# Optimization experiments

Hardware: AMD Instinct MI355X
Metric: run time of the kernel (lower is better)

Reference implementation:

```python
import jax, jax.numpy as jnp
import numpy as np

IN_F, OUT_F, K_MAX = 4096, 4096, 512
B, S = 8, 2048


def setup_inputs() -> dict:
    key = jax.random.key(0)
    kx, ku, kv = jax.random.split(key, 3)
    x = jax.random.normal(kx, (B, S, IN_F), dtype=jnp.float32)
    # kaiming_uniform_ with a=sqrt(5): bound = sqrt(6 / ((1 + a^2) * fan_in)) = sqrt(1/fan_in)
    bu = 1.0 / np.sqrt(IN_F)
    bv = 1.0 / np.sqrt(OUT_F)
    U = jax.random.uniform(ku, (IN_F, K_MAX), minval=-bu, maxval=bu, dtype=jnp.float32)
    V = jax.random.uniform(kv, (OUT_F, K_MAX), minval=-bv, maxval=bv, dtype=jnp.float32)
    s = jnp.ones((K_MAX,), dtype=jnp.float32)
    mask = jnp.ones((K_MAX,), dtype=jnp.bool_)
    return {"x": x, "U": U, "V": V, "s": s, "mask": mask}


def reference(x, U, V, s, mask):
    # s_masked = s * mask; W = V @ diag(s_masked) @ U^T; out = x @ W^T
    s_masked = s * mask.astype(s.dtype)            # [k]
    W = (V * s_masked[None, :]) @ U.T              # [out, in] (V @ diag(s) fused as column scale)
    return jnp.einsum('bsi,oi->bso', x, W)         # F.linear(x, W)
```

## Files before the change

kernel.cpp:

```cpp
#include <hip/hip_runtime.h>
#include <hip/hip_bf16.h>
#include <stdint.h>


typedef __attribute__((ext_vector_type(8))) short short8;
typedef __attribute__((ext_vector_type(4))) float f32x4;
typedef __attribute__((ext_vector_type(4))) unsigned int uint4v;


__device__ __forceinline__ unsigned short f2bf_rne(float f) {
    unsigned int u = __builtin_bit_cast(unsigned int, f);
    unsigned int r = u + 0x7fffu + ((u >> 16) & 1u);
    return (unsigned short)(r >> 16);
}

__device__ __forceinline__ unsigned int pk2bf(float a, float b) {
    unsigned int ua = __builtin_bit_cast(unsigned int, a);
    unsigned int ub = __builtin_bit_cast(unsigned int, b);
    ua = (ua + 0x8000u) >> 16;
    ub = (ub + 0x8000u) & 0xffff0000u;
    return ua | ub;
}

__device__ __forceinline__ void async_load16(const void* g, void* l) {
    __builtin_amdgcn_global_load_lds(
        (const __attribute__((address_space(1))) unsigned int*)g,
        (__attribute__((address_space(3))) unsigned int*)l,
        16, 0, 0);
}


__global__ void prep_u(const float* __restrict__ U, const float* __restrict__ S,
                       const int* __restrict__ Mask, unsigned short* __restrict__ Ut) {
    __shared__ float t[32][33];
    const int tx = threadIdx.x, ty = threadIdx.y;
    const int n0 = blockIdx.x * 32, k0 = blockIdx.y * 32;
#pragma unroll
    for (int i = 0; i < 4; ++i)
        t[ty + i * 8][tx] = U[(size_t)(k0 + ty + i * 8) * 512 + n0 + tx];
    __syncthreads();
#pragma unroll
    for (int i = 0; i < 4; ++i) {
        int n = n0 + ty + i * 8;
        float sm = S[n] * (Mask[n] != 0 ? 1.0f : 0.0f);
        Ut[(size_t)n * 4096 + k0 + tx] = f2bf_rne(t[tx][ty + i * 8] * sm);
    }
}

__global__ void prep_v(const float* __restrict__ V, unsigned short* __restrict__ Vb) {
    int i = blockIdx.x * blockDim.x + threadIdx.x;
    float4 f = ((const float4*)V)[i];
    ushort4 o;
    o.x = f2bf_rne(f.x); o.y = f2bf_rne(f.y);
    o.z = f2bf_rne(f.z); o.w = f2bf_rne(f.w);
    ((ushort4*)Vb)[i] = o;
}

__global__ __launch_bounds__(256, 2)
void gemm1_xu(const float* __restrict__ X, const unsigned short* __restrict__ Ut,
              unsigned short* __restrict__ Y) {
    const int tid  = threadIdx.x;
    const int lane = tid & 63;
    const int w    = tid >> 6;
    const int ln   = lane & 15;
    const int quad = lane >> 4;
    const int m0 = blockIdx.y * 128;
    const int n0 = blockIdx.x * 128;
    const int wm = (w >> 1) * 64;
    const int wn = (w & 1) * 64;

    __shared__ short8 As[1024];
    __shared__ short8 Bs[1024];

    f32x4 acc[4][4] = {};

    for (int kt = 0; kt < 4096; kt += 64) {
        __syncthreads();
#pragma unroll
        for (int i = 0; i < 4; ++i) {
            int cbase = i * 256 + w * 64;
            int c = cbase + lane;
            int kc = c >> 7, n = c & 127;
            async_load16(Ut + (size_t)(n0 + n) * 4096 + kt + kc * 8, (void*)&Bs[cbase]);
        }
#pragma unroll
        for (int i = 0; i < 4; ++i) {
            int c = i * 256 + tid;
            int kc = c >> 7, m = c & 127;
            const float* src = X + (size_t)(m0 + m) * 4096 + kt + kc * 8;
            float4 f0 = *(const float4*)(src);
            float4 f1 = *(const float4*)(src + 4);
            uint4v p;
            p.x = pk2bf(f0.x, f0.y); p.y = pk2bf(f0.z, f0.w);
            p.z = pk2bf(f1.x, f1.y); p.w = pk2bf(f1.z, f1.w);
            As[c] = __builtin_bit_cast(short8, p);
        }
        __syncthreads();
#pragma unroll
        for (int ks = 0; ks < 2; ++ks) {
            const int kc = ks * 4 + quad;
            short8 a[4], b[4];
#pragma unroll
            for (int t = 0; t < 4; ++t) {
                a[t] = As[kc * 128 + wm + t * 16 + ln];
                b[t] = Bs[kc * 128 + wn + t * 16 + ln];
            }
#pragma unroll
            for (int mt = 0; mt < 4; ++mt)
#pragma unroll
                for (int nt = 0; nt < 4; ++nt)
                    acc[mt][nt] = __builtin_amdgcn_mfma_f32_16x16x32_bf16(
                        a[mt], b[nt], acc[mt][nt], 0, 0, 0);
        }
    }
#pragma unroll
    for (int mt = 0; mt < 4; ++mt)
#pragma unroll
        for (int nt = 0; nt < 4; ++nt) {
            int col = n0 + wn + nt * 16 + ln;
#pragma unroll
            for (int r = 0; r < 4; ++r) {
                int row = m0 + wm + mt * 16 + quad * 4 + r;
                Y[(size_t)row * 512 + col] = f2bf_rne(acc[mt][nt][r]);
            }
        }
}

__global__ __launch_bounds__(256, 2)
void gemm2_yv(const unsigned short* __restrict__ Y, const unsigned short* __restrict__ Vb,
              float* __restrict__ Out) {
    const int tid  = threadIdx.x;
    const int lane = tid & 63;
    const int w    = tid >> 6;
    const int ln   = lane & 15;
    const int quad = lane >> 4;
    const int m0 = blockIdx.y * 128;
    const int n0 = blockIdx.x * 128;
    const int wm = (w >> 1) * 64;
    const int wn = (w & 1) * 64;

    __shared__ short8 As[1024];
    __shared__ short8 Bs[1024];

    f32x4 acc[4][4] = {};

    for (int kt = 0; kt < 512; kt += 64) {
        __syncthreads();
#pragma unroll
        for (int i = 0; i < 4; ++i) {
            int cbase = i * 256 + w * 64;
            int c = cbase + lane;
            int kc = c >> 7, r = c & 127;
            async_load16(Y  + (size_t)(m0 + r) * 512 + kt + kc * 8, (void*)&As[cbase]);
            async_load16(Vb + (size_t)(n0 + r) * 512 + kt + kc * 8, (void*)&Bs[cbase]);
        }
        __syncthreads();
#pragma unroll
        for (int ks = 0; ks < 2; ++ks) {
            const int kc = ks * 4 + quad;
            short8 a[4], b[4];
#pragma unroll
            for (int t = 0; t < 4; ++t) {
                a[t] = As[kc * 128 + wm + t * 16 + ln];
                b[t] = Bs[kc * 128 + wn + t * 16 + ln];
            }
#pragma unroll
            for (int mt = 0; mt < 4; ++mt)
#pragma unroll
                for (int nt = 0; nt < 4; ++nt)
                    acc[mt][nt] = __builtin_amdgcn_mfma_f32_16x16x32_bf16(
                        a[mt], b[nt], acc[mt][nt], 0, 0, 0);
        }
    }
#pragma unroll
    for (int mt = 0; mt < 4; ++mt)
#pragma unroll
        for (int nt = 0; nt < 4; ++nt) {
            int col = n0 + wn + nt * 16 + ln;
#pragma unroll
            for (int r = 0; r < 4; ++r) {
                int row = m0 + wm + mt * 16 + quad * 4 + r;
                Out[(size_t)row * 4096 + col] = acc[mt][nt][r];
            }
        }
}


extern "C" void kernel_launch(void* const* d_in, const int* in_sizes, int n_in,
                              void* d_out, int out_size, void* d_ws, size_t ws_size,
                              hipStream_t stream) {
    const float* X    = (const float*)d_in[0];
    const float* U    = (const float*)d_in[1];
    const float* V    = (const float*)d_in[2];
    const float* S    = (const float*)d_in[3];
    const int*   Mask = (const int*)d_in[4];

    char* ws = (char*)d_ws;
    unsigned short* Ut = (unsigned short*)ws;
    unsigned short* Vb = (unsigned short*)(ws + (size_t)512 * 4096 * 2);
    unsigned short* Yb = (unsigned short*)(ws + (size_t)512 * 4096 * 4);
    float* Out = (float*)d_out;

    prep_u<<<dim3(16, 128), dim3(32, 8), 0, stream>>>(U, S, Mask, Ut);
    prep_v<<<dim3(1024), dim3(512), 0, stream>>>(V, Vb);
    gemm1_xu<<<dim3(4, 128), dim3(256), 0, stream>>>(X, Ut, Yb);
    gemm2_yv<<<dim3(32, 128), dim3(256), 0, stream>>>(Yb, Vb, Out);
}
```

Measured before the change: 759.6 us.

## Pre-convert X to bf16 and double-buffer LDS in a unified GEMM kernel

Adds a separate prep_x pass that converts the fp32 activations to bf16, so GEMM1 can load both operands with async global-to-LDS copies instead of converting X inside the main loop. Both GEMMs now share one templated kernel that double-buffers shared memory, issuing the next tile's loads before computing the current one. This removes one barrier per iteration and overlaps loads with MFMA work. The cost is an extra full read of X plus a 128 MB bf16 write and read, and twice the LDS per block. If the workspace is too small, the output buffer is reused as scratch for X.

```diff
diff --git a/kernel.cpp b/kernel.cpp
--- a/kernel.cpp
+++ b/kernel.cpp
@@ -56,9 +56,22 @@
     ((ushort4*)Vb)[i] = o;
 }
 
+__global__ __launch_bounds__(256) void prep_x(const float* __restrict__ X,
+                                              unsigned short* __restrict__ Xb) {
+    size_t i = (size_t)blockIdx.x * 256 + threadIdx.x;
+    const float4* src = (const float4*)X;
+    float4 f0 = src[2 * i];
+    float4 f1 = src[2 * i + 1];
+    uint4v p;
+    p.x = pk2bf(f0.x, f0.y); p.y = pk2bf(f0.z, f0.w);
+    p.z = pk2bf(f1.x, f1.y); p.w = pk2bf(f1.z, f1.w);
+    ((uint4v*)Xb)[i] = p;
+}
+
+template <int K, bool OUT_BF16, int LDOUT>
 __global__ __launch_bounds__(256, 2)
-void gemm1_xu(const float* __restrict__ X, const unsigned short* __restrict__ Ut,
-              unsigned short* __restrict__ Y) {
+void gemm_bt(const unsigned short* __restrict__ A, const unsigned short* __restrict__ B,
+             void* __restrict__ Out) {
     const int tid  = threadIdx.x;
     const int lane = tid & 63;
     const int w    = tid >> 6;
@@ -69,41 +82,38 @@
     const int wm = (w >> 1) * 64;
     const int wn = (w & 1) * 64;
 
-    __shared__ short8 As[1024];
-    __shared__ short8 Bs[1024];
+    __shared__ short8 As[2][1024];
+    __shared__ short8 Bs[2][1024];
 
     f32x4 acc[4][4] = {};
 
-    for (int kt = 0; kt < 4096; kt += 64) {
-        __syncthreads();
+    constexpr int NT = K / 64;
+
+    auto stage = [&](int buf, int kt) {
 #pragma unroll
         for (int i = 0; i < 4; ++i) {
             int cbase = i * 256 + w * 64;
             int c = cbase + lane;
-            int kc = c >> 7, n = c & 127;
-            async_load16(Ut + (size_t)(n0 + n) * 4096 + kt + kc * 8, (void*)&Bs[cbase]);
+            int kc = c >> 7, r = c & 127;
+            async_load16(A + (size_t)(m0 + r) * K + kt + kc * 8, (void*)&As[buf][cbase]);
+            async_load16(B + (size_t)(n0 + r) * K + kt + kc * 8, (void*)&Bs[buf][cbase]);
         }
-#pragma unroll
-        for (int i = 0; i < 4; ++i) {
-            int c = i * 256 + tid;
-            int kc = c >> 7, m = c & 127;
-            const float* src = X + (size_t)(m0 + m) * 4096 + kt + kc * 8;
-            float4 f0 = *(const float4*)(src);
-            float4 f1 = *(const float4*)(src + 4);
-            uint4v p;
-            p.x = pk2bf(f0.x, f0.y); p.y = pk2bf(f0.z, f0.w);
-            p.z = pk2bf(f1.x, f1.y); p.w = pk2bf(f1.z, f1.w);
-            As[c] = __builtin_bit_cast(short8, p);
-        }
+    };
+
+    stage(0, 0);
+    int cur = 0;
+#pragma unroll 1
+    for (int t = 0; t < NT; ++t) {
         __syncthreads();
+        if (t + 1 < NT) stage(cur ^ 1, (t + 1) * 64);
 #pragma unroll
         for (int ks = 0; ks < 2; ++ks) {
             const int kc = ks * 4 + quad;
             short8 a[4], b[4];
 #pragma unroll
-            for (int t = 0; t < 4; ++t) {
-                a[t] = As[kc * 128 + wm + t * 16 + ln];
-                b[t] = Bs[kc * 128 + wn + t * 16 + ln];
+            for (int tt = 0; tt < 4; ++tt) {
+                a[tt] = As[cur][kc * 128 + wm + tt * 16 + ln];
+                b[tt] = Bs[cur][kc * 128 + wn + tt * 16 + ln];
             }
 #pragma unroll
             for (int mt = 0; mt < 4; ++mt)
@@ -112,7 +122,9 @@
                     acc[mt][nt] = __builtin_amdgcn_mfma_f32_16x16x32_bf16(
                         a[mt], b[nt], acc[mt][nt], 0, 0, 0);
         }
+        cur ^= 1;
     }
+
 #pragma unroll
     for (int mt = 0; mt < 4; ++mt)
 #pragma unroll
@@ -121,66 +133,10 @@
 #pragma unroll
             for (int r = 0; r < 4; ++r) {
                 int row = m0 + wm + mt * 16 + quad * 4 + r;
-                Y[(size_t)row * 512 + col] = f2bf_rne(acc[mt][nt][r]);
-            }
-        }
-}
-
-__global__ __launch_bounds__(256, 2)
-void gemm2_yv(const unsigned short* __restrict__ Y, const unsigned short* __restrict__ Vb,
-              float* __restrict__ Out) {
-    const int tid  = threadIdx.x;
-    const int lane = tid & 63;
-    const int w    = tid >> 6;
-    const int ln   = lane & 15;
-    const int quad = lane >> 4;
-    const int m0 = blockIdx.y * 128;
-    const int n0 = blockIdx.x * 128;
-    const int wm = (w >> 1) * 64;
-    const int wn = (w & 1) * 64;
-
-    __shared__ short8 As[1024];
-    __shared__ short8 Bs[1024];
-
-    f32x4 acc[4][4] = {};
-
-    for (int kt = 0; kt < 512; kt += 64) {
-        __syncthreads();
-#pragma unroll
-        for (int i = 0; i < 4; ++i) {
-            int cbase = i * 256 + w * 64;
-            int c = cbase + lane;
-            int kc = c >> 7, r = c & 127;
-            async_load16(Y  + (size_t)(m0 + r) * 512 + kt + kc * 8, (void*)&As[cbase]);
-            async_load16(Vb + (size_t)(n0 + r) * 512 + kt + kc * 8, (void*)&Bs[cbase]);
-        }
-        __syncthreads();
-#pragma unroll
-        for (int ks = 0; ks < 2; ++ks) {
-            const int kc = ks * 4 + quad;
-            short8 a[4], b[4];
-#pragma unroll
-            for (int t = 0; t < 4; ++t) {
-                a[t] = As[kc * 128 + wm + t * 16 + ln];
-                b[t] = Bs[kc * 128 + wn + t * 16 + ln];
-            }
-#pragma unroll
-            for (int mt = 0; mt < 4; ++mt)
-#pragma unroll
-                for (int nt = 0; nt < 4; ++nt)
-                    acc[mt][nt] = __builtin_amdgcn_mfma_f32_16x16x32_bf16(
-                        a[mt], b[nt], acc[mt][nt], 0, 0, 0);
-        }
-    }
-#pragma unroll
-    for (int mt = 0; mt < 4; ++mt)
-#pragma unroll
-        for (int nt = 0; nt < 4; ++nt) {
-            int col = n0 + wn + nt * 16 + ln;
-#pragma unroll
-            for (int r = 0; r < 4; ++r) {
-                int row = m0 + wm + mt * 16 + quad * 4 + r;
-                Out[(size_t)row * 4096 + col] = acc[mt][nt][r];
+                if constexpr (OUT_BF16)
+                    ((unsigned short*)Out)[(size_t)row * LDOUT + col] = f2bf_rne(acc[mt][nt][r]);
+                else
+                    ((float*)Out)[(size_t)row * LDOUT + col] = acc[mt][nt][r];
             }
         }
 }
@@ -196,13 +152,25 @@
     const int*   Mask = (const int*)d_in[4];
 
     char* ws = (char*)d_ws;
+    const size_t UT_B = (size_t)512 * 4096 * 2;
+    const size_t VB_B = (size_t)512 * 4096 * 2;
+    const size_t YB_B = (size_t)16384 * 512 * 2;
+    const size_t XB_B = (size_t)16384 * 4096 * 2;
+
     unsigned short* Ut = (unsigned short*)ws;
-    unsigned short* Vb = (unsigned short*)(ws + (size_t)512 * 4096 * 2);
-    unsigned short* Yb = (unsigned short*)(ws + (size_t)512 * 4096 * 4);
+    unsigned short* Vb = (unsigned short*)(ws + UT_B);
+    unsigned short* Yb = (unsigned short*)(ws + UT_B + VB_B);
     float* Out = (float*)d_out;
+
+    unsigned short* Xb;
+    if (ws_size >= UT_B + VB_B + YB_B + XB_B)
+        Xb = (unsigned short*)(ws + UT_B + VB_B + YB_B);
+    else
+        Xb = (unsigned short*)d_out;
 
     prep_u<<<dim3(16, 128), dim3(32, 8), 0, stream>>>(U, S, Mask, Ut);
     prep_v<<<dim3(1024), dim3(512), 0, stream>>>(V, Vb);
-    gemm1_xu<<<dim3(4, 128), dim3(256), 0, stream>>>(X, Ut, Yb);
-    gemm2_yv<<<dim3(32, 128), dim3(256), 0, stream>>>(Yb, Vb, Out);
+    prep_x<<<dim3(32768), dim3(256), 0, stream>>>(X, Xb);
+    gemm_bt<4096, true, 512><<<dim3(4, 128), dim3(256), 0, stream>>>(Xb, Ut, Yb);
+    gemm_bt<512, false, 4096><<<dim3(32, 128), dim3(256), 0, stream>>>(Yb, Vb, Out);
 }
```

Result: slower. 781.6 us (+2.9%).
